# Kernel tuning notes

Measured on AMD Instinct MI355X. Metric: run time of the kernel, lower is better.

Reference implementation:

```python
import jax, jax.numpy as jnp
import numpy as np

DIM = 1024
H = 16
DH = DIM // H
EPS = 1e-5
NEG = -1e38


def _layernorm(x, g, b):
    m = jnp.mean(x, axis=-1, keepdims=True)
    v = jnp.mean((x - m) ** 2, axis=-1, keepdims=True)
    return (x - m) / jnp.sqrt(v + EPS) * g + b


def setup_inputs() -> dict:
    key = jax.random.key(0)
    ks = jax.random.split(key, 12)
    B, Nq, Nk = 4, 1024, 1024
    Q = jax.random.normal(ks[0], (B, Nq, DIM), dtype=jnp.float32)
    K = jax.random.normal(ks[1], (B, Nk, DIM), dtype=jnp.float32)
    V = jax.random.normal(ks[2], (B, Nk, DIM), dtype=jnp.float32)
    mask_Q = jax.random.randint(ks[3], (B, Nq), 0, 2).astype(jnp.bool_)
    mask_K = jax.random.randint(ks[4], (B, Nk), 0, 2).astype(jnp.bool_)
    s = 0.02
    Wq = jax.random.normal(ks[5], (DIM, DIM), dtype=jnp.float32) * s
    Wk = jax.random.normal(ks[6], (DIM, DIM), dtype=jnp.float32) * s
    Wv = jax.random.normal(ks[7], (DIM, DIM), dtype=jnp.float32) * s
    Wo = jax.random.normal(ks[8], (DIM, DIM), dtype=jnp.float32) * s
    ln1_g = jnp.ones((DIM,), jnp.float32); ln1_b = jnp.zeros((DIM,), jnp.float32)
    ln2_g = jnp.ones((DIM,), jnp.float32); ln2_b = jnp.zeros((DIM,), jnp.float32)
    return {"Q": Q, "K": K, "V": V, "Wq": Wq, "Wk": Wk, "Wv": Wv, "Wo": Wo,
            "ln1_g": ln1_g, "ln1_b": ln1_b, "ln2_g": ln2_g, "ln2_b": ln2_b,
            "mask_Q": mask_Q, "mask_K": mask_K}


def reference(Q, K, V, Wq, Wk, Wv, Wo, ln1_g, ln1_b, ln2_g, ln2_b, mask_Q, mask_K):
    B, Nq, _ = Q.shape
    Nk = K.shape[1]
    # zero out padded tokens before projection (mask_tensors)
    Qm = jnp.where(mask_Q[..., None], 0.0, Q)
    Km = jnp.where(mask_K[..., None], 0.0, K)
    Vm = jnp.where(mask_K[..., None], 0.0, V)
    # projections (bias=False); torch Linear stores W as [out, in]
    Qp = Qm @ Wq.T
    Kp = Km @ Wk.T
    Vp = Vm @ Wv.T
    # split heads: [B, N, H, DH]
    Qh = Qp.reshape(B, Nq, H, DH)
    Kh = Kp.reshape(B, Nk, H, DH)
    Vh = Vp.reshape(B, Nk, H, DH)
    # NOTE: original scales by sqrt(dim_V), not sqrt(head_dim)
    scores = jnp.einsum('bqhd,bkhd->bhqk', Qh, Kh) / jnp.sqrt(jnp.float32(DIM))
    pad = mask_Q[:, None, :, None] | mask_K[:, None, None, :]  # [B,1,Nq,Nk]
    A = jax.nn.softmax(jnp.where(pad, NEG, scores), axis=-1)
    A = jnp.where(pad, 0.0, A)  # post-softmax masked_fill (dropout = identity in eval)
    O = jnp.einsum('bhqk,bkhd->bqhd', A, Vh).reshape(B, Nq, DIM)
    mq = mask_Q[..., None]
    # residual uses the PROJECTED Q
    O = Qp + O
    O = jnp.where(mq, 0.0, _layernorm(O, ln1_g, ln1_b))
    # masked fc_o then exact (non-tanh) GELU; gelu(0)=0 so masking commutes
    h = jnp.where(mq, 0.0, O @ Wo.T)
    O = O + jax.nn.gelu(h, approximate=False)
    O = jnp.where(mq, 0.0, _layernorm(O, ln2_g, ln2_b))
    return O
```

## Files before the change

### kernel.cpp

```cpp
#include <hip/hip_runtime.h>

#define NTOK 4096
#define AST 72

typedef _Float16 half4v __attribute__((ext_vector_type(4)));
typedef _Float16 half8 __attribute__((ext_vector_type(8)));
typedef float floatx4 __attribute__((ext_vector_type(4)));

__device__ __forceinline__ half8 cvt8(float4 a, float4 b) {
  half8 h;
  h[0] = (_Float16)a.x; h[1] = (_Float16)a.y; h[2] = (_Float16)a.z; h[3] = (_Float16)a.w;
  h[4] = (_Float16)b.x; h[5] = (_Float16)b.y; h[6] = (_Float16)b.z; h[7] = (_Float16)b.w;
  return h;
}

#if defined(__has_builtin)
#if __has_builtin(__builtin_amdgcn_global_load_lds)
#define HAS_GLL 1
#endif
#endif

#ifdef HAS_GLL
#define STAGE16(gp, lp)                                                        \
  __builtin_amdgcn_global_load_lds(                                           \
      (const __attribute__((address_space(1))) void*)(gp),                     \
      (__attribute__((address_space(3))) void*)(lp), 16, 0, 0)
#else
#define STAGE16(gp, lp)                                                        \
  do { *(half8*)((_Float16*)(lp) + lane * 8) = *(const half8*)(gp); } while (0)
#endif

__device__ __forceinline__ int mask_is_bytes(const int* p) {
  int bad = 0;
#pragma unroll
  for (int i = 0; i < 64; i++) bad |= (((unsigned int)p[i]) > 1u);
  return bad;
}

__global__ __launch_bounds__(256) void mask_prep(
    const int* __restrict__ srcQ, const int* __restrict__ srcK,
    int* __restrict__ dstQ, int* __restrict__ dstK)
{
  const int t = blockIdx.x * 256 + threadIdx.x;
  const int bq = mask_is_bytes(srcQ);
  const int bk = mask_is_bytes(srcK);
  dstQ[t] = bq ? (int)((const unsigned char*)srcQ)[t] : srcQ[t];
  dstK[t] = bk ? (int)((const unsigned char*)srcK)[t] : srcK[t];
}

__global__ __launch_bounds__(256) void cvt_all(
    const float* __restrict__ Q, const float* __restrict__ K, const float* __restrict__ V,
    const float* __restrict__ Wq, const float* __restrict__ Wk, const float* __restrict__ Wv,
    const float* __restrict__ Wo,
    _Float16* __restrict__ Xq, _Float16* __restrict__ Xk, _Float16* __restrict__ Xv,
    _Float16* __restrict__ Wqh, _Float16* __restrict__ Wkh, _Float16* __restrict__ Wvh,
    _Float16* __restrict__ Woh)
{
  const int blk = blockIdx.x;
  const float* src; _Float16* dst; size_t off;
  if      (blk < 2048) { src = Q;  dst = Xq;  off = (size_t)blk * 2048; }
  else if (blk < 4096) { src = K;  dst = Xk;  off = (size_t)(blk - 2048) * 2048; }
  else if (blk < 6144) { src = V;  dst = Xv;  off = (size_t)(blk - 4096) * 2048; }
  else if (blk < 6656) { src = Wq; dst = Wqh; off = (size_t)(blk - 6144) * 2048; }
  else if (blk < 7168) { src = Wk; dst = Wkh; off = (size_t)(blk - 6656) * 2048; }
  else if (blk < 7680) { src = Wv; dst = Wvh; off = (size_t)(blk - 7168) * 2048; }
  else                 { src = Wo; dst = Woh; off = (size_t)(blk - 7680) * 2048; }
  const size_t i = off + (size_t)threadIdx.x * 8;
  const float4 a = *(const float4*)(src + i);
  const float4 b = *(const float4*)(src + i + 4);
  *(half8*)(dst + i) = cvt8(a, b);
}

#define GEMM97_CORE(AH, BH)                                                    \
  __shared__ _Float16 sA[128 * 32];                                            \
  __shared__ _Float16 sB[128 * 32];                                            \
  const int t = threadIdx.x;                                                   \
  const int bn = blockIdx.x, bm = blockIdx.y;                                  \
  const int lane = t & 63, wv = t >> 6, quad = lane >> 4, l16 = lane & 15;     \
  const int wm = wv & 1, wn = wv >> 1;                                         \
  const int srow = wv * 32 + (lane >> 2);                                      \
  const int scol = (lane & 3) * 8;                                             \
  floatx4 acc[4][4] = {};                                                      \
  const _Float16* gA = AH + (size_t)(bm * 128 + srow) * 1024 + scol;           \
  const _Float16* gB = BH + (size_t)(bn * 128 + srow) * 1024 + scol;           \
  for (int kt = 0; kt < 32; kt++) {                                            \
    __syncthreads();                                                           \
    STAGE16(gA + kt * 32,         &sA[(wv * 32) * 32]);                        \
    STAGE16(gA + kt * 32 + 16384, &sA[(wv * 32 + 16) * 32]);                   \
    STAGE16(gB + kt * 32,         &sB[(wv * 32) * 32]);                        \
    STAGE16(gB + kt * 32 + 16384, &sB[(wv * 32 + 16) * 32]);                   \
    __syncthreads();                                                           \
    half8 af[4], bf[4];                                                        \
    _Pragma("unroll")                                                          \
    for (int s = 0; s < 4; s++)                                                \
      af[s] = *(const half8*)&sA[(wm * 64 + s * 16 + l16) * 32 + quad * 8];    \
    _Pragma("unroll")                                                          \
    for (int u = 0; u < 4; u++)                                                \
      bf[u] = *(const half8*)&sB[(wn * 64 + u * 16 + l16) * 32 + quad * 8];    \
    _Pragma("unroll")                                                          \
    for (int s = 0; s < 4; s++)                                                \
      _Pragma("unroll")                                                        \
      for (int u = 0; u < 4; u++)                                              \
        acc[s][u] = __builtin_amdgcn_mfma_f32_16x16x32_f16(af[s], bf[u],       \
                                                           acc[s][u], 0, 0, 0); \
  }

__global__ __launch_bounds__(256) void qkv_gemm(
    const _Float16* __restrict__ Xq, const _Float16* __restrict__ Xk,
    const _Float16* __restrict__ Xv,
    const _Float16* __restrict__ Wqh, const _Float16* __restrict__ Wkh,
    const _Float16* __restrict__ Wvh,
    const int* __restrict__ mQ, const int* __restrict__ mK,
    _Float16* __restrict__ Qh, _Float16* __restrict__ Kh, _Float16* __restrict__ Vh)
{
  const int z = blockIdx.z;
  const _Float16* AH = (z == 0) ? Xq : (z == 1) ? Xk : Xv;
  const _Float16* BH = (z == 0) ? Wqh : (z == 1) ? Wkh : Wvh;
  const int* msk = (z == 0) ? mQ : mK;
  _Float16* out = (z == 0) ? Qh : (z == 1) ? Kh : Vh;
  GEMM97_CORE(AH, BH)
#pragma unroll
  for (int s = 0; s < 4; s++)
#pragma unroll
    for (int rr = 0; rr < 4; rr++) {
      const int row = bm * 128 + wm * 64 + s * 16 + quad * 4 + rr;
      const int m = msk[row];
#pragma unroll
      for (int u = 0; u < 4; u++)
        out[(size_t)row * 1024 + bn * 128 + wn * 64 + u * 16 + l16] =
            m ? (_Float16)0.0f : (_Float16)acc[s][u][rr];
    }
}

__global__ __launch_bounds__(256) void gemm_wo(
    const _Float16* __restrict__ AH, const _Float16* __restrict__ BH,
    const float* __restrict__ X1, float* __restrict__ O2)
{
  __shared__ _Float16 sA[128 * 32];
  __shared__ _Float16 sB[64 * 32];
  const int t = threadIdx.x;
  const int bn = blockIdx.x, bm = blockIdx.y;
  const int lane = t & 63, wv = t >> 6, quad = lane >> 4, l16 = lane & 15;
  const int srowA = wv * 32 + (lane >> 2);
  const int srowB = wv * 16 + (lane >> 2);
  const int scol = (lane & 3) * 8;
  floatx4 acc[2][4] = {};
  const _Float16* gA = AH + (size_t)(bm * 128 + srowA) * 1024 + scol;
  const _Float16* gB = BH + (size_t)(bn * 64 + srowB) * 1024 + scol;
  for (int kt = 0; kt < 32; kt++) {
    __syncthreads();
    STAGE16(gA + kt * 32,         &sA[(wv * 32) * 32]);
    STAGE16(gA + kt * 32 + 16384, &sA[(wv * 32 + 16) * 32]);
    STAGE16(gB + kt * 32,         &sB[(wv * 16) * 32]);
    __syncthreads();
    half8 af[2], bf[4];
#pragma unroll
    for (int s = 0; s < 2; s++)
      af[s] = *(const half8*)&sA[(wv * 32 + s * 16 + l16) * 32 + quad * 8];
#pragma unroll
    for (int u = 0; u < 4; u++)
      bf[u] = *(const half8*)&sB[(u * 16 + l16) * 32 + quad * 8];
#pragma unroll
    for (int s = 0; s < 2; s++)
#pragma unroll
      for (int u = 0; u < 4; u++)
        acc[s][u] = __builtin_amdgcn_mfma_f32_16x16x32_f16(af[s], bf[u],
                                                           acc[s][u], 0, 0, 0);
  }
#pragma unroll
  for (int s = 0; s < 2; s++)
#pragma unroll
    for (int rr = 0; rr < 4; rr++) {
      const int row = bm * 128 + wv * 32 + s * 16 + quad * 4 + rr;
#pragma unroll
      for (int u = 0; u < 4; u++) {
        const size_t idx = (size_t)row * 1024 + bn * 64 + u * 16 + l16;
        const float hv = acc[s][u][rr];
        const float ge = 0.5f * hv * (1.0f + erff(hv * 0.70710678118654752f));
        O2[idx] = X1[idx] + ge;
      }
    }
}

__global__ __launch_bounds__(256) void v_transpose(
    const _Float16* __restrict__ Vh, _Float16* __restrict__ Vt)
{
  __shared__ _Float16 sT[64 * AST];
  const int t = threadIdx.x;
  const int kt = blockIdx.x, bh = blockIdx.y;
  const int b = bh >> 4, h = bh & 15;
  const int r = t >> 2, c0 = (t & 3) * 16;
  const _Float16* src = Vh + (size_t)(b * 1024 + kt * 64 + r) * 1024 + h * 64 + c0;
  *(half8*)&sT[r * AST + c0] = *(const half8*)src;
  *(half8*)&sT[r * AST + c0 + 8] = *(const half8*)(src + 8);
  __syncthreads();
  half8 o0, o1;
#pragma unroll
  for (int j = 0; j < 8; j++) o0[j] = sT[(c0 + j) * AST + r];
#pragma unroll
  for (int j = 0; j < 8; j++) o1[j] = sT[(c0 + 8 + j) * AST + r];
  _Float16* dst = Vt + ((size_t)bh * 64 + r) * 1024 + kt * 64 + c0;
  *(half8*)dst = o0;
  *(half8*)(dst + 8) = o1;
}

__global__ __launch_bounds__(256) void attn_mfma3(
    const _Float16* __restrict__ Qh, const _Float16* __restrict__ Kh,
    const _Float16* __restrict__ Vt, const int* __restrict__ maskQ,
    const int* __restrict__ maskK, float* __restrict__ O1)
{
  __shared__ _Float16 sK[64 * AST];
  __shared__ _Float16 sV[64 * AST];
  __shared__ _Float16 sQP[64 * AST];
  __shared__ float bias[1024];

  const int t = threadIdx.x;
  const int qt = blockIdx.x, bh = blockIdx.y;
  const int b = bh >> 4, h = bh & 15;
  const int q0 = qt * 64;
  const size_t base = (size_t)b * 1024;
  const int wv = t >> 6, lane = t & 63, quad = lane >> 4, l16 = lane & 15;
  const int r = t >> 2, c0 = (t & 3) * 16;

  for (int i = t; i < 1024; i += 256)
    bias[i] = maskK[b * 1024 + i] ? -1e30f : 0.0f;

  {
    const _Float16* qp = Qh + (base + q0 + r) * 1024 + h * 64 + c0;
    *(half8*)&sQP[r * AST + c0] = *(const half8*)qp;
    *(half8*)&sQP[r * AST + c0 + 8] = *(const half8*)(qp + 8);
  }
  __syncthreads();

  const half8 bq0 = *(const half8*)&sQP[(wv * 16 + l16) * AST + quad * 8];
  const half8 bq1 = *(const half8*)&sQP[(wv * 16 + l16) * AST + 32 + quad * 8];

  float m_i = -1e30f, l_i = 0.0f;
  floatx4 acc_o[4] = {};

  for (int kt = 0; kt < 16; kt++) {
    __syncthreads();
    {
      const _Float16* kp = Kh + (base + kt * 64 + r) * 1024 + h * 64 + c0;
      const _Float16* vp = Vt + ((size_t)bh * 64 + r) * 1024 + kt * 64 + c0;
      const half8 k0v = *(const half8*)kp;
      const half8 k1v = *(const half8*)(kp + 8);
      const half8 v0v = *(const half8*)vp;
      const half8 v1v = *(const half8*)(vp + 8);
      *(half8*)&sK[r * AST + c0] = k0v;
      *(half8*)&sK[r * AST + c0 + 8] = k1v;
      *(half8*)&sV[r * AST + c0] = v0v;
      *(half8*)&sV[r * AST + c0 + 8] = v1v;
    }
    __syncthreads();

    floatx4 s[4] = {};
#pragma unroll
    for (int mt = 0; mt < 4; mt++) {
      const half8 ak0 = *(const half8*)&sK[(mt * 16 + l16) * AST + quad * 8];
      const half8 ak1 = *(const half8*)&sK[(mt * 16 + l16) * AST + 32 + quad * 8];
      s[mt] = __builtin_amdgcn_mfma_f32_16x16x32_f16(ak0, bq0, s[mt], 0, 0, 0);
      s[mt] = __builtin_amdgcn_mfma_f32_16x16x32_f16(ak1, bq1, s[mt], 0, 0, 0);
    }
#pragma unroll
    for (int mt = 0; mt < 4; mt++) {
      const float4 b4 = *(const float4*)&bias[kt * 64 + mt * 16 + quad * 4];
      s[mt][0] = s[mt][0] * 0.03125f + b4.x;
      s[mt][1] = s[mt][1] * 0.03125f + b4.y;
      s[mt][2] = s[mt][2] * 0.03125f + b4.z;
      s[mt][3] = s[mt][3] * 0.03125f + b4.w;
    }

    float mx = -1e30f;
#pragma unroll
    for (int mt = 0; mt < 4; mt++)
      mx = fmaxf(mx, fmaxf(fmaxf(s[mt][0], s[mt][1]), fmaxf(s[mt][2], s[mt][3])));
    mx = fmaxf(mx, __shfl_xor(mx, 16));
    mx = fmaxf(mx, __shfl_xor(mx, 32));
    const float mn = fmaxf(m_i, mx);
    const float alpha = __expf(m_i - mn);
    m_i = mn;

    float rsum = 0.0f;
#pragma unroll
    for (int mt = 0; mt < 4; mt++)
#pragma unroll
      for (int rr = 0; rr < 4; rr++) {
        const float sv = s[mt][rr];
        const float p = (sv <= -1e20f) ? 0.0f : __expf(sv - mn);
        s[mt][rr] = p;
        rsum += p;
      }
    rsum += __shfl_xor(rsum, 16);
    rsum += __shfl_xor(rsum, 32);
    l_i = l_i * alpha + rsum;

    float al[4];
#pragma unroll
    for (int rr = 0; rr < 4; rr++) al[rr] = __shfl(alpha, quad * 4 + rr);
#pragma unroll
    for (int nt = 0; nt < 4; nt++)
#pragma unroll
      for (int rr = 0; rr < 4; rr++)
        acc_o[nt][rr] *= al[rr];

#pragma unroll
    for (int mt = 0; mt < 4; mt++) {
      half4v pv;
      pv[0] = (_Float16)s[mt][0]; pv[1] = (_Float16)s[mt][1];
      pv[2] = (_Float16)s[mt][2]; pv[3] = (_Float16)s[mt][3];
      *(half4v*)&sQP[(wv * 16 + l16) * AST + mt * 16 + quad * 4] = pv;
    }

    const half8 ap0 = *(const half8*)&sQP[(wv * 16 + l16) * AST + quad * 8];
    const half8 ap1 = *(const half8*)&sQP[(wv * 16 + l16) * AST + 32 + quad * 8];
#pragma unroll
    for (int nt = 0; nt < 4; nt++) {
      const half8 bv0 = *(const half8*)&sV[(nt * 16 + l16) * AST + quad * 8];
      const half8 bv1 = *(const half8*)&sV[(nt * 16 + l16) * AST + 32 + quad * 8];
      acc_o[nt] = __builtin_amdgcn_mfma_f32_16x16x32_f16(ap0, bv0, acc_o[nt], 0, 0, 0);
      acc_o[nt] = __builtin_amdgcn_mfma_f32_16x16x32_f16(ap1, bv1, acc_o[nt], 0, 0, 0);
    }
  }

  float il[4];
#pragma unroll
  for (int rr = 0; rr < 4; rr++) {
    const float lq = __shfl(l_i, quad * 4 + rr);
    il[rr] = (lq > 0.0f) ? 1.0f / lq : 0.0f;
  }
#pragma unroll
  for (int rr = 0; rr < 4; rr++) {
    const int row = q0 + wv * 16 + quad * 4 + rr;
    const int mq = maskQ[b * 1024 + row];
#pragma unroll
    for (int nt = 0; nt < 4; nt++) {
      const size_t gi = (base + row) * 1024 + h * 64 + nt * 16 + l16;
      O1[gi] = mq ? 0.0f : ((float)Qh[gi] + acc_o[nt][rr] * il[rr]);
    }
  }
}

__device__ __forceinline__ void ln_stats(float4 x, int t, float* mean, float* rinv) {
  float s = x.x + x.y + x.z + x.w;
  float s2 = x.x * x.x + x.y * x.y + x.z * x.z + x.w * x.w;
#pragma unroll
  for (int off = 32; off >= 1; off >>= 1) { s += __shfl_xor(s, off); s2 += __shfl_xor(s2, off); }
  __shared__ float red[8];
  __shared__ float sm[2];
  const int wv = t >> 6, lane = t & 63;
  if (lane == 0) { red[wv] = s; red[4 + wv] = s2; }
  __syncthreads();
  if (t == 0) {
    const float S = red[0] + red[1] + red[2] + red[3];
    const float S2 = red[4] + red[5] + red[6] + red[7];
    const float m = S * (1.0f / 1024.0f);
    const float v = S2 * (1.0f / 1024.0f) - m * m;
    sm[0] = m; sm[1] = rsqrtf(v + 1e-5f);
  }
  __syncthreads();
  *mean = sm[0]; *rinv = sm[1];
}

__global__ __launch_bounds__(256) void ln_f32(
    const float* __restrict__ X, const float* __restrict__ g,
    const float* __restrict__ bta, const int* __restrict__ mask,
    float* __restrict__ out)
{
  const int rr = blockIdx.x, t = threadIdx.x, c = 4 * t;
  const float4 x = *(const float4*)&X[(size_t)rr * 1024 + c];
  float mean, ri;
  ln_stats(x, t, &mean, &ri);
  const int msk = mask[rr];
  const float4 gg = *(const float4*)&g[c];
  const float4 bb = *(const float4*)&bta[c];
  float4 o;
  o.x = msk ? 0.f : (x.x - mean) * ri * gg.x + bb.x;
  o.y = msk ? 0.f : (x.y - mean) * ri * gg.y + bb.y;
  o.z = msk ? 0.f : (x.z - mean) * ri * gg.z + bb.z;
  o.w = msk ? 0.f : (x.w - mean) * ri * gg.w + bb.w;
  *(float4*)&out[(size_t)rr * 1024 + c] = o;
}

__global__ __launch_bounds__(256) void ln_f32h(
    const float* __restrict__ X, const float* __restrict__ g,
    const float* __restrict__ bta, const int* __restrict__ mask,
    float* __restrict__ out, _Float16* __restrict__ outh)
{
  const int rr = blockIdx.x, t = threadIdx.x, c = 4 * t;
  const float4 x = *(const float4*)&X[(size_t)rr * 1024 + c];
  float mean, ri;
  ln_stats(x, t, &mean, &ri);
  const int msk = mask[rr];
  const float4 gg = *(const float4*)&g[c];
  const float4 bb = *(const float4*)&bta[c];
  float4 o;
  o.x = msk ? 0.f : (x.x - mean) * ri * gg.x + bb.x;
  o.y = msk ? 0.f : (x.y - mean) * ri * gg.y + bb.y;
  o.z = msk ? 0.f : (x.z - mean) * ri * gg.z + bb.z;
  o.w = msk ? 0.f : (x.w - mean) * ri * gg.w + bb.w;
  const size_t idx = (size_t)rr * 1024 + c;
  *(float4*)&out[idx] = o;
  half4v hh;
  hh[0] = (_Float16)o.x; hh[1] = (_Float16)o.y;
  hh[2] = (_Float16)o.z; hh[3] = (_Float16)o.w;
  *(half4v*)&outh[idx] = hh;
}

extern "C" void kernel_launch(void* const* d_in, const int* in_sizes, int n_in,
                              void* d_out, int out_size, void* d_ws, size_t ws_size,
                              hipStream_t stream)
{
  const float* Q  = (const float*)d_in[0];
  const float* K  = (const float*)d_in[1];
  const float* V  = (const float*)d_in[2];
  const float* Wq = (const float*)d_in[3];
  const float* Wk = (const float*)d_in[4];
  const float* Wv = (const float*)d_in[5];
  const float* Wo = (const float*)d_in[6];
  const float* g1 = (const float*)d_in[7];
  const float* b1 = (const float*)d_in[8];
  const float* g2 = (const float*)d_in[9];
  const float* b2 = (const float*)d_in[10];
  float* out = (float*)d_out;

  char* base = (char*)d_ws;
  const size_t MB_ = 1024 * 1024;
  _Float16* Xq  = (_Float16*)(base +  0 * MB_);
  _Float16* Xk  = (_Float16*)(base +  8 * MB_);
  _Float16* Xv  = (_Float16*)(base + 16 * MB_);
  _Float16* Wqh = (_Float16*)(base + 24 * MB_);
  _Float16* Wkh = (_Float16*)(base + 26 * MB_);
  _Float16* Wvh = (_Float16*)(base + 28 * MB_);
  _Float16* Woh = (_Float16*)(base + 30 * MB_);
  _Float16* Qh  = (_Float16*)(base + 32 * MB_);
  _Float16* Kh  = (_Float16*)(base + 40 * MB_);
  _Float16* Vh  = (_Float16*)(base + 48 * MB_);
  _Float16* Vt  = (_Float16*)(base + 56 * MB_);
  float*    O1  = (float*)(base + 64 * MB_);
  int*      mQ  = (int*)(base + 80 * MB_);
  int*      mK  = mQ + NTOK;
  float*    X1  = (float*)(base + 0 * MB_);
  _Float16* X1h = (_Float16*)(base + 16 * MB_);
  float*    O2  = (float*)(base + 32 * MB_);

  const dim3 bb(256);
  mask_prep<<<dim3(16), bb, 0, stream>>>((const int*)d_in[11], (const int*)d_in[12], mQ, mK);
  cvt_all<<<dim3(8192), bb, 0, stream>>>(Q, K, V, Wq, Wk, Wv, Wo,
                                         Xq, Xk, Xv, Wqh, Wkh, Wvh, Woh);
  qkv_gemm<<<dim3(8, 32, 3), bb, 0, stream>>>(Xq, Xk, Xv, Wqh, Wkh, Wvh,
                                              mQ, mK, Qh, Kh, Vh);
  v_transpose<<<dim3(16, 64), bb, 0, stream>>>(Vh, Vt);
  attn_mfma3<<<dim3(16, 64), bb, 0, stream>>>(Qh, Kh, Vt, mQ, mK, O1);
  ln_f32h<<<dim3(4096), bb, 0, stream>>>(O1, g1, b1, mQ, X1, X1h);
  gemm_wo<<<dim3(16, 32), bb, 0, stream>>>(X1h, Woh, X1, O2);
  ln_f32<<<dim3(4096), bb, 0, stream>>>(O2, g2, b2, mQ, out);
}
```

Baseline: 261.0 us.

## Fuse V transpose into QKV GEMM epilogue and double attention query tile

The QKV GEMM epilogue for V now transposes through shared memory and writes Vt directly, which removes the separate v_transpose kernel and its extra read/write of V. K is pre-scaled by log2(e)/sqrt(1024), so the attention softmax can use exp2f without a per-score multiply, and the explicit masked-score check is dropped. The attention kernel now handles 128 queries per block, two 16-row subtiles per wave, so each K/V tile loaded into LDS is reused twice as often. The costs are more registers, 34KB of extra shared memory in the QKV GEMM, and half as many attention blocks.

New measurement: 280.3 us. 7.4% more time.

```diff
diff --git a/kernel.cpp b/kernel.cpp
--- a/kernel.cpp
+++ b/kernel.cpp
@@ -2,10 +2,13 @@
 
 #define NTOK 4096
 #define AST 72
+#define TST 136
 
 typedef _Float16 half4v __attribute__((ext_vector_type(4)));
 typedef _Float16 half8 __attribute__((ext_vector_type(8)));
 typedef float floatx4 __attribute__((ext_vector_type(4)));
+
+#define KSCALE 0.045084220027780106f
 
 __device__ __forceinline__ half8 cvt8(float4 a, float4 b) {
   half8 h;
@@ -111,25 +114,54 @@
     const _Float16* __restrict__ Wqh, const _Float16* __restrict__ Wkh,
     const _Float16* __restrict__ Wvh,
     const int* __restrict__ mQ, const int* __restrict__ mK,
-    _Float16* __restrict__ Qh, _Float16* __restrict__ Kh, _Float16* __restrict__ Vh)
-{
+    _Float16* __restrict__ Qh, _Float16* __restrict__ Kh, _Float16* __restrict__ Vt)
+{
+  __shared__ _Float16 sT[128 * TST];
   const int z = blockIdx.z;
   const _Float16* AH = (z == 0) ? Xq : (z == 1) ? Xk : Xv;
   const _Float16* BH = (z == 0) ? Wqh : (z == 1) ? Wkh : Wvh;
   const int* msk = (z == 0) ? mQ : mK;
-  _Float16* out = (z == 0) ? Qh : (z == 1) ? Kh : Vh;
   GEMM97_CORE(AH, BH)
-#pragma unroll
-  for (int s = 0; s < 4; s++)
-#pragma unroll
-    for (int rr = 0; rr < 4; rr++) {
-      const int row = bm * 128 + wm * 64 + s * 16 + quad * 4 + rr;
-      const int m = msk[row];
-#pragma unroll
-      for (int u = 0; u < 4; u++)
-        out[(size_t)row * 1024 + bn * 128 + wn * 64 + u * 16 + l16] =
-            m ? (_Float16)0.0f : (_Float16)acc[s][u][rr];
-    }
+
+  if (z == 2) {
+#pragma unroll
+    for (int s = 0; s < 4; s++)
+#pragma unroll
+      for (int rr = 0; rr < 4; rr++) {
+        const int kloc = wm * 64 + s * 16 + quad * 4 + rr;
+        const int m = msk[bm * 128 + kloc];
+#pragma unroll
+        for (int u = 0; u < 4; u++) {
+          const int dloc = wn * 64 + u * 16 + l16;
+          sT[dloc * TST + kloc] = m ? (_Float16)0.0f : (_Float16)acc[s][u][rr];
+        }
+      }
+    __syncthreads();
+    const int b = bm >> 3;
+    const int kb = (bm & 7) * 128 + (t & 15) * 8;
+#pragma unroll
+    for (int p = 0; p < 8; p++) {
+      const int dloc = p * 16 + (t >> 4);
+      const int gcol = bn * 128 + dloc;
+      const half8 v = *(const half8*)&sT[dloc * TST + (t & 15) * 8];
+      _Float16* dst = Vt + ((size_t)(b * 16 + (gcol >> 6)) * 64 + (gcol & 63)) * 1024 + kb;
+      *(half8*)dst = v;
+    }
+  } else {
+    _Float16* out = (z == 0) ? Qh : Kh;
+    const float sc = (z == 0) ? 1.0f : KSCALE;
+#pragma unroll
+    for (int s = 0; s < 4; s++)
+#pragma unroll
+      for (int rr = 0; rr < 4; rr++) {
+        const int row = bm * 128 + wm * 64 + s * 16 + quad * 4 + rr;
+        const int m = msk[row];
+#pragma unroll
+        for (int u = 0; u < 4; u++)
+          out[(size_t)row * 1024 + bn * 128 + wn * 64 + u * 16 + l16] =
+              m ? (_Float16)0.0f : (_Float16)(acc[s][u][rr] * sc);
+      }
+  }
 }
 
 __global__ __launch_bounds__(256) void gemm_wo(
@@ -182,42 +214,20 @@
     }
 }
 
-__global__ __launch_bounds__(256) void v_transpose(
-    const _Float16* __restrict__ Vh, _Float16* __restrict__ Vt)
-{
-  __shared__ _Float16 sT[64 * AST];
-  const int t = threadIdx.x;
-  const int kt = blockIdx.x, bh = blockIdx.y;
-  const int b = bh >> 4, h = bh & 15;
-  const int r = t >> 2, c0 = (t & 3) * 16;
-  const _Float16* src = Vh + (size_t)(b * 1024 + kt * 64 + r) * 1024 + h * 64 + c0;
-  *(half8*)&sT[r * AST + c0] = *(const half8*)src;
-  *(half8*)&sT[r * AST + c0 + 8] = *(const half8*)(src + 8);
-  __syncthreads();
-  half8 o0, o1;
-#pragma unroll
-  for (int j = 0; j < 8; j++) o0[j] = sT[(c0 + j) * AST + r];
-#pragma unroll
-  for (int j = 0; j < 8; j++) o1[j] = sT[(c0 + 8 + j) * AST + r];
-  _Float16* dst = Vt + ((size_t)bh * 64 + r) * 1024 + kt * 64 + c0;
-  *(half8*)dst = o0;
-  *(half8*)(dst + 8) = o1;
-}
-
-__global__ __launch_bounds__(256) void attn_mfma3(
+__global__ __launch_bounds__(256) void attn_mfma4(
     const _Float16* __restrict__ Qh, const _Float16* __restrict__ Kh,
     const _Float16* __restrict__ Vt, const int* __restrict__ maskQ,
     const int* __restrict__ maskK, float* __restrict__ O1)
 {
   __shared__ _Float16 sK[64 * AST];
   __shared__ _Float16 sV[64 * AST];
-  __shared__ _Float16 sQP[64 * AST];
+  __shared__ _Float16 sQP[128 * AST];
   __shared__ float bias[1024];
 
   const int t = threadIdx.x;
   const int qt = blockIdx.x, bh = blockIdx.y;
   const int b = bh >> 4, h = bh & 15;
-  const int q0 = qt * 64;
+  const int q0 = qt * 128;
   const size_t base = (size_t)b * 1024;
   const int wv = t >> 6, lane = t & 63, quad = lane >> 4, l16 = lane & 15;
   const int r = t >> 2, c0 = (t & 3) * 16;
@@ -226,17 +236,24 @@
     bias[i] = maskK[b * 1024 + i] ? -1e30f : 0.0f;
 
   {
-    const _Float16* qp = Qh + (base + q0 + r) * 1024 + h * 64 + c0;
-    *(half8*)&sQP[r * AST + c0] = *(const half8*)qp;
-    *(half8*)&sQP[r * AST + c0 + 8] = *(const half8*)(qp + 8);
+    const int r2 = t >> 1, cs = (t & 1) * 32;
+    const _Float16* qp = Qh + (base + q0 + r2) * 1024 + h * 64 + cs;
+    *(half8*)&sQP[r2 * AST + cs]      = *(const half8*)qp;
+    *(half8*)&sQP[r2 * AST + cs + 8]  = *(const half8*)(qp + 8);
+    *(half8*)&sQP[r2 * AST + cs + 16] = *(const half8*)(qp + 16);
+    *(half8*)&sQP[r2 * AST + cs + 24] = *(const half8*)(qp + 24);
   }
   __syncthreads();
 
-  const half8 bq0 = *(const half8*)&sQP[(wv * 16 + l16) * AST + quad * 8];
-  const half8 bq1 = *(const half8*)&sQP[(wv * 16 + l16) * AST + 32 + quad * 8];
-
-  float m_i = -1e30f, l_i = 0.0f;
-  floatx4 acc_o[4] = {};
+  half8 bq[2][2];
+#pragma unroll
+  for (int qs = 0; qs < 2; qs++) {
+    bq[qs][0] = *(const half8*)&sQP[(wv * 32 + qs * 16 + l16) * AST + quad * 8];
+    bq[qs][1] = *(const half8*)&sQP[(wv * 32 + qs * 16 + l16) * AST + 32 + quad * 8];
+  }
+
+  float m_i[2] = {-1e30f, -1e30f}, l_i[2] = {0.0f, 0.0f};
+  floatx4 acc_o[2][4] = {};
 
   for (int kt = 0; kt < 16; kt++) {
     __syncthreads();
@@ -254,89 +271,99 @@
     }
     __syncthreads();
 
-    floatx4 s[4] = {};
+    floatx4 s[2][4] = {};
 #pragma unroll
     for (int mt = 0; mt < 4; mt++) {
       const half8 ak0 = *(const half8*)&sK[(mt * 16 + l16) * AST + quad * 8];
       const half8 ak1 = *(const half8*)&sK[(mt * 16 + l16) * AST + 32 + quad * 8];
-      s[mt] = __builtin_amdgcn_mfma_f32_16x16x32_f16(ak0, bq0, s[mt], 0, 0, 0);
-      s[mt] = __builtin_amdgcn_mfma_f32_16x16x32_f16(ak1, bq1, s[mt], 0, 0, 0);
+#pragma unroll
+      for (int qs = 0; qs < 2; qs++) {
+        s[qs][mt] = __builtin_amdgcn_mfma_f32_16x16x32_f16(ak0, bq[qs][0], s[qs][mt], 0, 0, 0);
+        s[qs][mt] = __builtin_amdgcn_mfma_f32_16x16x32_f16(ak1, bq[qs][1], s[qs][mt], 0, 0, 0);
+      }
     }
 #pragma unroll
     for (int mt = 0; mt < 4; mt++) {
       const float4 b4 = *(const float4*)&bias[kt * 64 + mt * 16 + quad * 4];
-      s[mt][0] = s[mt][0] * 0.03125f + b4.x;
-      s[mt][1] = s[mt][1] * 0.03125f + b4.y;
-      s[mt][2] = s[mt][2] * 0.03125f + b4.z;
-      s[mt][3] = s[mt][3] * 0.03125f + b4.w;
-    }
-
-    float mx = -1e30f;
-#pragma unroll
-    for (int mt = 0; mt < 4; mt++)
-      mx = fmaxf(mx, fmaxf(fmaxf(s[mt][0], s[mt][1]), fmaxf(s[mt][2], s[mt][3])));
-    mx = fmaxf(mx, __shfl_xor(mx, 16));
-    mx = fmaxf(mx, __shfl_xor(mx, 32));
-    const float mn = fmaxf(m_i, mx);
-    const float alpha = __expf(m_i - mn);
-    m_i = mn;
-
-    float rsum = 0.0f;
-#pragma unroll
-    for (int mt = 0; mt < 4; mt++)
-#pragma unroll
-      for (int rr = 0; rr < 4; rr++) {
-        const float sv = s[mt][rr];
-        const float p = (sv <= -1e20f) ? 0.0f : __expf(sv - mn);
-        s[mt][rr] = p;
-        rsum += p;
-      }
-    rsum += __shfl_xor(rsum, 16);
-    rsum += __shfl_xor(rsum, 32);
-    l_i = l_i * alpha + rsum;
-
-    float al[4];
-#pragma unroll
-    for (int rr = 0; rr < 4; rr++) al[rr] = __shfl(alpha, quad * 4 + rr);
-#pragma unroll
-    for (int nt = 0; nt < 4; nt++)
-#pragma unroll
-      for (int rr = 0; rr < 4; rr++)
-        acc_o[nt][rr] *= al[rr];
-
-#pragma unroll
-    for (int mt = 0; mt < 4; mt++) {
-      half4v pv;
-      pv[0] = (_Float16)s[mt][0]; pv[1] = (_Float16)s[mt][1];
-      pv[2] = (_Float16)s[mt][2]; pv[3] = (_Float16)s[mt][3];
-      *(half4v*)&sQP[(wv * 16 + l16) * AST + mt * 16 + quad * 4] = pv;
-    }
-
-    const half8 ap0 = *(const half8*)&sQP[(wv * 16 + l16) * AST + quad * 8];
-    const half8 ap1 = *(const half8*)&sQP[(wv * 16 + l16) * AST + 32 + quad * 8];
-#pragma unroll
-    for (int nt = 0; nt < 4; nt++) {
-      const half8 bv0 = *(const half8*)&sV[(nt * 16 + l16) * AST + quad * 8];
-      const half8 bv1 = *(const half8*)&sV[(nt * 16 + l16) * AST + 32 + quad * 8];
-      acc_o[nt] = __builtin_amdgcn_mfma_f32_16x16x32_f16(ap0, bv0, acc_o[nt], 0, 0, 0);
-      acc_o[nt] = __builtin_amdgcn_mfma_f32_16x16x32_f16(ap1, bv1, acc_o[nt], 0, 0, 0);
-    }
-  }
-
-  float il[4];
-#pragma unroll
-  for (int rr = 0; rr < 4; rr++) {
-    const float lq = __shfl(l_i, quad * 4 + rr);
-    il[rr] = (lq > 0.0f) ? 1.0f / lq : 0.0f;
-  }
-#pragma unroll
-  for (int rr = 0; rr < 4; rr++) {
-    const int row = q0 + wv * 16 + quad * 4 + rr;
-    const int mq = maskQ[b * 1024 + row];
-#pragma unroll
-    for (int nt = 0; nt < 4; nt++) {
-      const size_t gi = (base + row) * 1024 + h * 64 + nt * 16 + l16;
-      O1[gi] = mq ? 0.0f : ((float)Qh[gi] + acc_o[nt][rr] * il[rr]);
+#pragma unroll
+      for (int qs = 0; qs < 2; qs++) {
+        s[qs][mt][0] += b4.x; s[qs][mt][1] += b4.y;
+        s[qs][mt][2] += b4.z; s[qs][mt][3] += b4.w;
+      }
+    }
+
+#pragma unroll
+    for (int qs = 0; qs < 2; qs++) {
+      float mx = -1e30f;
+#pragma unroll
+      for (int mt = 0; mt < 4; mt++)
+        mx = fmaxf(mx, fmaxf(fmaxf(s[qs][mt][0], s[qs][mt][1]),
+                             fmaxf(s[qs][mt][2], s[qs][mt][3])));
+      mx = fmaxf(mx, __shfl_xor(mx, 16));
+      mx = fmaxf(mx, __shfl_xor(mx, 32));
+      const float mn = fmaxf(m_i[qs], mx);
+      const float alpha = exp2f(m_i[qs] - mn);
+      m_i[qs] = mn;
+
+      float rsum = 0.0f;
+#pragma unroll
+      for (int mt = 0; mt < 4; mt++)
+#pragma unroll
+        for (int rr = 0; rr < 4; rr++) {
+          const float p = exp2f(s[qs][mt][rr] - mn);
+          s[qs][mt][rr] = p;
+          rsum += p;
+        }
+      rsum += __shfl_xor(rsum, 16);
+      rsum += __shfl_xor(rsum, 32);
+      l_i[qs] = l_i[qs] * alpha + rsum;
+
+      float al[4];
+#pragma unroll
+      for (int rr = 0; rr < 4; rr++) al[rr] = __shfl(alpha, quad * 4 + rr);
+#pragma unroll
+      for (int nt = 0; nt < 4; nt++)
+#pragma unroll
+        for (int rr = 0; rr < 4; rr++)
+          acc_o[qs][nt][rr] *= al[rr];
+
+#pragma unroll
+      for (int mt = 0; mt < 4; mt++) {
+        half4v pv;
+        pv[0] = (_Float16)s[qs][mt][0]; pv[1] = (_Float16)s[qs][mt][1];
+        pv[2] = (_Float16)s[qs][mt][2]; pv[3] = (_Float16)s[qs][mt][3];
+        *(half4v*)&sQP[(wv * 32 + qs * 16 + l16) * AST + mt * 16 + quad * 4] = pv;
+      }
+
+      const half8 ap0 = *(const half8*)&sQP[(wv * 32 + qs * 16 + l16) * AST + quad * 8];
+      const half8 ap1 = *(const half8*)&sQP[(wv * 32 + qs * 16 + l16) * AST + 32 + quad * 8];
+#pragma unroll
+      for (int nt = 0; nt < 4; nt++) {
+        const half8 bv0 = *(const half8*)&sV[(nt * 16 + l16) * AST + quad * 8];
+        const half8 bv1 = *(const half8*)&sV[(nt * 16 + l16) * AST + 32 + quad * 8];
+        acc_o[qs][nt] = __builtin_amdgcn_mfma_f32_16x16x32_f16(ap0, bv0, acc_o[qs][nt], 0, 0, 0);
+        acc_o[qs][nt] = __builtin_amdgcn_mfma_f32_16x16x32_f16(ap1, bv1, acc_o[qs][nt], 0, 0, 0);
+      }
+    }
+  }
+
+#pragma unroll
+  for (int qs = 0; qs < 2; qs++) {
+    float il[4];
+#pragma unroll
+    for (int rr = 0; rr < 4; rr++) {
+      const float lq = __shfl(l_i[qs], quad * 4 + rr);
+      il[rr] = (lq > 0.0f) ? 1.0f / lq : 0.0f;
+    }
+#pragma unroll
+    for (int rr = 0; rr < 4; rr++) {
+      const int row = q0 + wv * 32 + qs * 16 + quad * 4 + rr;
+      const int mq = maskQ[b * 1024 + row];
+#pragma unroll
+      for (int nt = 0; nt < 4; nt++) {
+        const size_t gi = (base + row) * 1024 + h * 64 + nt * 16 + l16;
+        O1[gi] = mq ? 0.0f : ((float)Qh[gi] + acc_o[qs][nt][rr] * il[rr]);
+      }
     }
   }
 }
@@ -435,8 +462,7 @@
   _Float16* Woh = (_Float16*)(base + 30 * MB_);
   _Float16* Qh  = (_Float16*)(base + 32 * MB_);
   _Float16* Kh  = (_Float16*)(base + 40 * MB_);
-  _Float16* Vh  = (_Float16*)(base + 48 * MB_);
-  _Float16* Vt  = (_Float16*)(base + 56 * MB_);
+  _Float16* Vt  = (_Float16*)(base + 48 * MB_);
   float*    O1  = (float*)(base + 64 * MB_);
   int*      mQ  = (int*)(base + 80 * MB_);
   int*      mK  = mQ + NTOK;
@@ -449,9 +475,8 @@
   cvt_all<<<dim3(8192), bb, 0, stream>>>(Q, K, V, Wq, Wk, Wv, Wo,
                                          Xq, Xk, Xv, Wqh, Wkh, Wvh, Woh);
   qkv_gemm<<<dim3(8, 32, 3), bb, 0, stream>>>(Xq, Xk, Xv, Wqh, Wkh, Wvh,
-                                              mQ, mK, Qh, Kh, Vh);
-  v_transpose<<<dim3(16, 64), bb, 0, stream>>>(Vh, Vt);
-  attn_mfma3<<<dim3(16, 64), bb, 0, stream>>>(Qh, Kh, Vt, mQ, mK, O1);
+                                              mQ, mK, Qh, Kh, Vt);
+  attn_mfma4<<<dim3(8, 64), bb, 0, stream>>>(Qh, Kh, Vt, mQ, mK, O1);
   ln_f32h<<<dim3(4096), bb, 0, stream>>>(O1, g1, b1, mQ, X1, X1h);
   gemm_wo<<<dim3(16, 32), bb, 0, stream>>>(X1h, Woh, X1, O2);
   ln_f32<<<dim3(4096), bb, 0, stream>>>(O2, g2, b2, mQ, out);
```
